# Kernel tuning notes

Hardware: AMD Instinct MI355X
Metric: run time of the kernel (lower is better)

The kernel has to match this reference:

```python
import jax, jax.numpy as jnp
import numpy as np

B, N, L = 2, 2048, 2048
DQ, DKV, H, WF = 1024, 1024, 16, 4
HD = DQ // H
EPS = 1e-5


def _ln(x, g, b):
    m = jnp.mean(x, axis=-1, keepdims=True)
    v = jnp.mean(jnp.square(x - m), axis=-1, keepdims=True)
    return (x - m) * jax.lax.rsqrt(v + EPS) * g + b


def setup_inputs() -> dict:
    key = jax.random.key(0)
    ks = jax.random.split(key, 12)
    s = 0.02
    return {
        "x_q": jax.random.normal(ks[0], (B, N, DQ), jnp.float32),
        "x_kv": jax.random.normal(ks[1], (B, L, DKV), jnp.float32),
        "qn_g": jnp.ones((DQ,), jnp.float32),
        "qn_b": jnp.zeros((DQ,), jnp.float32),
        "kvn_g": jnp.ones((DKV,), jnp.float32),
        "kvn_b": jnp.zeros((DKV,), jnp.float32),
        "Wq": jax.random.normal(ks[2], (DQ, DQ), jnp.float32) * s,
        "bq": jnp.zeros((DQ,), jnp.float32),
        "Wk": jax.random.normal(ks[3], (DQ, DKV), jnp.float32) * s,
        "bk": jnp.zeros((DQ,), jnp.float32),
        "Wv": jax.random.normal(ks[4], (DQ, DKV), jnp.float32) * s,
        "bv": jnp.zeros((DQ,), jnp.float32),
        "Wo": jax.random.normal(ks[5], (DQ, DQ), jnp.float32) * s,
        "bo": jnp.zeros((DQ,), jnp.float32),
        "n2_g": jnp.ones((DQ,), jnp.float32),
        "n2_b": jnp.zeros((DQ,), jnp.float32),
        "W1": jax.random.normal(ks[6], (WF * DQ, DQ), jnp.float32) * s,
        "b1": jnp.zeros((WF * DQ,), jnp.float32),
        "W2": jax.random.normal(ks[7], (DQ, WF * DQ), jnp.float32) * s,
        "b2": jnp.zeros((DQ,), jnp.float32),
    }


def reference(x_q, x_kv, qn_g, qn_b, kvn_g, kvn_b, Wq, bq, Wk, bk, Wv, bv,
              Wo, bo, n2_g, n2_b, W1, b1, W2, b2):
    # projections (torch Linear: x @ W.T + b)
    q = (_ln(x_q, qn_g, qn_b) @ Wq.T + bq).reshape(B, N, H, HD)
    kvn = _ln(x_kv, kvn_g, kvn_b)
    k = (kvn @ Wk.T + bk).reshape(B, L, H, HD)
    v = (kvn @ Wv.T + bv).reshape(B, L, H, HD)

    # attention with softmax-1: exp(s)/(1 + sum exp(s)), numerically stable
    scale = 1.0 / jnp.sqrt(jnp.float32(HD))
    s = jnp.einsum("bnhd,blhd->bhnl", q, k) * scale  # [B,H,N,L]
    m = jnp.max(s, axis=-1, keepdims=True)
    m = jnp.maximum(m, 0.0)  # include the implicit zero logit of softmax-1
    p = jnp.exp(s - m)
    denom = jnp.sum(p, axis=-1, keepdims=True) + jnp.exp(-m)
    attn = p / denom
    attn_out = jnp.einsum("bhnl,blhd->bnhd", attn, v).reshape(B, N, DQ)

    # residual + out proj
    x = x_q + (attn_out @ Wo.T + bo)
    # residual MLP (GELU, exact/erf as torch nn.GELU default)
    h = jax.nn.gelu(_ln(x, n2_g, n2_b) @ W1.T + b1, approximate=False)
    x = x + (h @ W2.T + b2)
    return x
```

## Files before the change

kernel.cpp:

```cpp
#include <hip/hip_runtime.h>
#include <hip/hip_bf16.h>
#include <stdint.h>

#define DEV __device__ __forceinline__

typedef unsigned short ushort_t;
typedef __attribute__((ext_vector_type(8))) short bf16x8;
typedef __attribute__((ext_vector_type(4))) float f32x4;

DEV ushort_t f2bf(float f) {
  union { float f; uint32_t u; } v; v.f = f;
  uint32_t r = v.u + 0x7FFFu + ((v.u >> 16) & 1u);
  return (ushort_t)(r >> 16);
}

DEV void gload_lds16(const void* gp, void* lp) {
  __builtin_amdgcn_global_load_lds(
      (__attribute__((address_space(1))) void*)(void*)(uintptr_t)gp,
      (__attribute__((address_space(3))) void*)lp, 16, 0, 0);
}

__global__ __launch_bounds__(256) void cvt_all(
    const float* __restrict__ Wq, const float* __restrict__ Wk,
    const float* __restrict__ Wv, const float* __restrict__ Wo,
    const float* __restrict__ W1, const float* __restrict__ W2,
    ushort_t* __restrict__ WqB, ushort_t* __restrict__ WKVB,
    ushort_t* __restrict__ WoB, ushort_t* __restrict__ W1B,
    ushort_t* __restrict__ W2B) {
  int i = blockIdx.x * 256 + threadIdx.x;
  const float* src; ushort_t* dst; int j;
  if (i < 262144)            { src = Wq; dst = WqB;           j = i; }
  else if (i < 524288)       { src = Wk; dst = WKVB;          j = i - 262144; }
  else if (i < 786432)       { src = Wv; dst = WKVB + 1048576; j = i - 524288; }
  else if (i < 1048576)      { src = Wo; dst = WoB;           j = i - 786432; }
  else if (i < 2097152)      { src = W1; dst = W1B;           j = i - 1048576; }
  else                       { src = W2; dst = W2B;           j = i - 2097152; }
  float4 v = ((const float4*)src)[j];
  ushort4 o;
  o.x = f2bf(v.x); o.y = f2bf(v.y); o.z = f2bf(v.z); o.w = f2bf(v.w);
  ((ushort4*)dst)[j] = o;
}

DEV void ln_row(const float* __restrict__ x, const float* __restrict__ g,
                const float* __restrict__ be, ushort_t* __restrict__ out, int row) {
  const int t = threadIdx.x;
  const float4 v = ((const float4*)(x + (size_t)row * 1024))[t];
  float s = v.x + v.y + v.z + v.w;
  float sq = v.x * v.x + v.y * v.y + v.z * v.z + v.w * v.w;
#pragma unroll
  for (int d = 1; d < 64; d <<= 1) { s += __shfl_xor(s, d); sq += __shfl_xor(sq, d); }
  __shared__ float sm[8];
  const int w = t >> 6, lane = t & 63;
  if (lane == 0) { sm[w * 2] = s; sm[w * 2 + 1] = sq; }
  __syncthreads();
  s = sm[0] + sm[2] + sm[4] + sm[6];
  sq = sm[1] + sm[3] + sm[5] + sm[7];
  const float mean = s * (1.f / 1024.f);
  const float var = sq * (1.f / 1024.f) - mean * mean;
  const float rstd = rsqrtf(var + 1e-5f);
  const float4 gv = ((const float4*)g)[t];
  const float4 bv = ((const float4*)be)[t];
  ushort4 o;
  o.x = f2bf((v.x - mean) * rstd * gv.x + bv.x);
  o.y = f2bf((v.y - mean) * rstd * gv.y + bv.y);
  o.z = f2bf((v.z - mean) * rstd * gv.z + bv.z);
  o.w = f2bf((v.w - mean) * rstd * gv.w + bv.w);
  ((ushort4*)(out + (size_t)row * 1024))[t] = o;
}

__global__ __launch_bounds__(256) void ln_bf16(const float* __restrict__ x,
                                               const float* __restrict__ g,
                                               const float* __restrict__ be,
                                               ushort_t* __restrict__ out) {
  ln_row(x, g, be, out, blockIdx.x);
}

__global__ __launch_bounds__(256) void ln_fused(
    const float* __restrict__ x_q, const float* __restrict__ x_kv,
    const float* __restrict__ qg, const float* __restrict__ qb,
    const float* __restrict__ kg, const float* __restrict__ kb,
    ushort_t* __restrict__ oq, ushort_t* __restrict__ okv) {
  const int r = blockIdx.x;
  if (r < 4096) ln_row(x_q, qg, qb, oq, r);
  else ln_row(x_kv, kg, kb, okv, r - 4096);
}

enum { EPI_BF16 = 0, EPI_KV = 1, EPI_RESID = 2, EPI_GELU = 3 };

template <int TN, int EPI>
__global__ __launch_bounds__(256, 2) void gemm_bt(
    const ushort_t* __restrict__ A,
    const ushort_t* __restrict__ Wb,
    const float* __restrict__ bias,
    const float* __restrict__ bias2,
    const float* __restrict__ resid,
    void* __restrict__ outp, void* __restrict__ outp2,
    int M, int N, int K) {
  constexpr int NI = (TN == 128) ? 4 : 2;
  __shared__ ushort_t As[128 * 64];
  __shared__ ushort_t Bs[TN * 64];
  const int t = threadIdx.x;
  const int w = t >> 6, lane = t & 63;
  const int qd = lane >> 4, ql = lane & 15;
  const int m0 = blockIdx.y * 128, n0 = blockIdx.x * TN;
  const int wm = (TN == 128) ? (w >> 1) * 64 : w * 32;
  const int wn = (TN == 128) ? (w & 1) * 64 : 0;
  const int sw = ql & 7;

  f32x4 acc[NI][4] = {};

  for (int k0 = 0; k0 < K; k0 += 64) {
#pragma unroll
    for (int p = 0; p < 4; p++) {
      int n = p * 256 + t, row = n >> 3, c = (n & 7) ^ (row & 7);
      gload_lds16(A + (size_t)(m0 + row) * K + k0 + c * 8, &As[n * 8]);
    }
#pragma unroll
    for (int p = 0; p < TN / 32; p++) {
      int n = p * 256 + t, row = n >> 3, c = (n & 7) ^ (row & 7);
      gload_lds16(Wb + (size_t)(n0 + row) * K + k0 + c * 8, &Bs[n * 8]);
    }
    __syncthreads();
#pragma unroll
    for (int ks = 0; ks < 2; ks++) {
      bf16x8 af[NI], bf[4];
#pragma unroll
      for (int i = 0; i < NI; i++)
        af[i] = *(const bf16x8*)&As[(wm + i * 16 + ql) * 64 + ((ks * 4 + qd) ^ sw) * 8];
#pragma unroll
      for (int j = 0; j < 4; j++)
        bf[j] = *(const bf16x8*)&Bs[(wn + j * 16 + ql) * 64 + ((ks * 4 + qd) ^ sw) * 8];
#pragma unroll
      for (int i = 0; i < NI; i++)
#pragma unroll
        for (int j = 0; j < 4; j++)
          acc[i][j] = __builtin_amdgcn_mfma_f32_16x16x32_bf16(af[i], bf[j], acc[i][j], 0, 0, 0);
    }
    __syncthreads();
  }

#pragma unroll
  for (int i = 0; i < NI; i++) {
    const int mr = m0 + wm + i * 16 + qd * 4;
#pragma unroll
    for (int j = 0; j < 4; j++) {
      const int col = n0 + wn + j * 16 + ql;
      f32x4 v = acc[i][j];
      if constexpr (EPI == EPI_BF16) {
        const float bb = bias[col];
        ushort_t* o = (ushort_t*)outp;
#pragma unroll
        for (int r = 0; r < 4; r++) o[(size_t)(mr + r) * N + col] = f2bf(v[r] + bb);
      } else if constexpr (EPI == EPI_KV) {
        if (col < 1024) {
          const float bb = bias[col];
          ushort_t* o = (ushort_t*)outp;
#pragma unroll
          for (int r = 0; r < 4; r++) o[(size_t)(mr + r) * 1024 + col] = f2bf(v[r] + bb);
        } else {
          const int vc = col - 1024;
          const float bb = bias2[vc];
          const int h = vc >> 6, d = vc & 63;
          const int b = mr >> 11, l0 = mr & 2047;
          ushort4 pk;
          pk.x = f2bf(v[0] + bb); pk.y = f2bf(v[1] + bb);
          pk.z = f2bf(v[2] + bb); pk.w = f2bf(v[3] + bb);
          *(ushort4*)((ushort_t*)outp2 + ((((size_t)b * 16 + h) * 64 + d) * 2048 + l0)) = pk;
        }
      } else if constexpr (EPI == EPI_RESID) {
        const float bb = bias[col];
        float* o = (float*)outp;
#pragma unroll
        for (int r = 0; r < 4; r++) {
          size_t idx = (size_t)(mr + r) * N + col;
          o[idx] = resid[idx] + v[r] + bb;
        }
      } else {
        const float bb = bias[col];
        ushort_t* o = (ushort_t*)outp;
#pragma unroll
        for (int r = 0; r < 4; r++) {
          float x = v[r] + bb;
          float gx = 0.5f * x * (1.0f + erff(x * 0.70710678118654752f));
          o[(size_t)(mr + r) * N + col] = f2bf(gx);
        }
      }
    }
  }
}

__global__ __launch_bounds__(256, 2) void flash_attn(const ushort_t* __restrict__ Qg,
                                                     const ushort_t* __restrict__ Kg,
                                                     const ushort_t* __restrict__ VTg,
                                                     ushort_t* __restrict__ Og) {
  __shared__ ushort_t Qs[128 * 64];
  __shared__ ushort_t Ks[2][64 * 64];
  __shared__ ushort_t Vs[2][64 * 64];
  __shared__ ushort_t Ps[128 * 64];
  const int t = threadIdx.x, w = t >> 6, lane = t & 63;
  const int qd = lane >> 4, ql = lane & 15;
  const int bh = blockIdx.y, b = bh >> 4, h = bh & 15;
  const int n0 = blockIdx.x * 128;
  const ushort_t* Qp = Qg + ((size_t)b * 2048 + n0) * 1024 + h * 64;
  const ushort_t* Kp = Kg + (size_t)b * 2048 * 1024 + h * 64;
  const ushort_t* Vp = VTg + (size_t)bh * 64 * 2048;
  const int sw = ql & 7;

#pragma unroll
  for (int p = 0; p < 4; p++) {
    int n = p * 256 + t, row = n >> 3, c = (n & 7) ^ (row & 7);
    gload_lds16(Qp + (size_t)row * 1024 + c * 8, &Qs[n * 8]);
  }
#pragma unroll
  for (int p = 0; p < 2; p++) {
    int n = p * 256 + t, row = n >> 3, c = (n & 7) ^ (row & 7);
    gload_lds16(Kp + (size_t)row * 1024 + c * 8, &Ks[0][n * 8]);
    gload_lds16(Vp + (size_t)row * 2048 + c * 8, &Vs[0][n * 8]);
  }
  __syncthreads();

  bf16x8 aq[2][2];
#pragma unroll
  for (int i = 0; i < 2; i++)
#pragma unroll
    for (int ks = 0; ks < 2; ks++)
      aq[i][ks] = *(const bf16x8*)&Qs[(w * 32 + i * 16 + ql) * 64 + ((ks * 4 + qd) ^ sw) * 8];

  f32x4 accO[2][4] = {};
  float lro[2][4] = {};

  int cur = 0;
  for (int lt = 0; lt < 32; ++lt) {
    if (lt + 1 < 32) {
      const int l0n = (lt + 1) * 64;
#pragma unroll
      for (int p = 0; p < 2; p++) {
        int n = p * 256 + t, row = n >> 3, c = (n & 7) ^ (row & 7);
        gload_lds16(Kp + (size_t)(l0n + row) * 1024 + c * 8, &Ks[1 ^ cur][n * 8]);
        gload_lds16(Vp + (size_t)row * 2048 + l0n + c * 8, &Vs[1 ^ cur][n * 8]);
      }
    }
    const ushort_t* Kc = Ks[cur];
    const ushort_t* Vc = Vs[cur];

    f32x4 accS[2][4] = {};
#pragma unroll
    for (int ks = 0; ks < 2; ks++) {
      bf16x8 bk[4];
#pragma unroll
      for (int j = 0; j < 4; j++)
        bk[j] = *(const bf16x8*)&Kc[(j * 16 + ql) * 64 + ((ks * 4 + qd) ^ sw) * 8];
#pragma unroll
      for (int i = 0; i < 2; i++)
#pragma unroll
        for (int j = 0; j < 4; j++)
          accS[i][j] = __builtin_amdgcn_mfma_f32_16x16x32_bf16(aq[i][ks], bk[j], accS[i][j], 0, 0, 0);
    }

#pragma unroll
    for (int i = 0; i < 2; i++)
#pragma unroll
      for (int j = 0; j < 4; j++)
#pragma unroll
        for (int r = 0; r < 4; r++) {
          float p_ = __expf(accS[i][j][r] * 0.125f);
          accS[i][j][r] = p_;
          lro[i][r] += p_;
        }

#pragma unroll
    for (int i = 0; i < 2; i++)
#pragma unroll
      for (int j = 0; j < 4; j++) {
        const int col = j * 16 + ql;
#pragma unroll
        for (int r = 0; r < 4; r++) {
          const int row = w * 32 + i * 16 + qd * 4 + r;
          Ps[row * 64 + (((col >> 3) ^ (row & 7)) * 8) + (col & 7)] = f2bf(accS[i][j][r]);
        }
      }

#pragma unroll
    for (int ks = 0; ks < 2; ks++) {
      bf16x8 ap[2], bv[4];
#pragma unroll
      for (int i = 0; i < 2; i++)
        ap[i] = *(const bf16x8*)&Ps[(w * 32 + i * 16 + ql) * 64 + ((ks * 4 + qd) ^ sw) * 8];
#pragma unroll
      for (int jo = 0; jo < 4; jo++)
        bv[jo] = *(const bf16x8*)&Vc[(jo * 16 + ql) * 64 + ((ks * 4 + qd) ^ sw) * 8];
#pragma unroll
      for (int i = 0; i < 2; i++)
#pragma unroll
        for (int jo = 0; jo < 4; jo++)
          accO[i][jo] = __builtin_amdgcn_mfma_f32_16x16x32_bf16(ap[i], bv[jo], accO[i][jo], 0, 0, 0);
    }

    __syncthreads();
    cur ^= 1;
  }

#pragma unroll
  for (int i = 0; i < 2; i++)
#pragma unroll
    for (int r = 0; r < 4; r++) {
      float l = lro[i][r];
#pragma unroll
      for (int d = 1; d < 16; d <<= 1) l += __shfl_xor(l, d);
      const float inv = 1.0f / (l + 1.0f);
      const int row = n0 + w * 32 + i * 16 + qd * 4 + r;
#pragma unroll
      for (int jo = 0; jo < 4; jo++)
        Og[((size_t)b * 2048 + row) * 1024 + h * 64 + jo * 16 + ql] =
            f2bf(accO[i][jo][r] * inv);
    }
}

extern "C" void kernel_launch(void* const* d_in, const int* in_sizes, int n_in,
                              void* d_out, int out_size, void* d_ws, size_t ws_size,
                              hipStream_t stream) {
  const float* x_q = (const float*)d_in[0];
  const float* x_kv = (const float*)d_in[1];
  const float* qn_g = (const float*)d_in[2];
  const float* qn_b = (const float*)d_in[3];
  const float* kvn_g = (const float*)d_in[4];
  const float* kvn_b = (const float*)d_in[5];
  const float* Wq = (const float*)d_in[6];
  const float* bq = (const float*)d_in[7];
  const float* Wk = (const float*)d_in[8];
  const float* bk = (const float*)d_in[9];
  const float* Wv = (const float*)d_in[10];
  const float* bv = (const float*)d_in[11];
  const float* Wo = (const float*)d_in[12];
  const float* bo = (const float*)d_in[13];
  const float* n2_g = (const float*)d_in[14];
  const float* n2_b = (const float*)d_in[15];
  const float* W1 = (const float*)d_in[16];
  const float* b1 = (const float*)d_in[17];
  const float* W2 = (const float*)d_in[18];
  const float* b2 = (const float*)d_in[19];

  char* ws = (char*)d_ws;
  const size_t MB = 1ull << 20;
  ushort_t* WqB = (ushort_t*)(ws + 0 * MB);
  ushort_t* WKVB = (ushort_t*)(ws + 2 * MB);
  ushort_t* WoB = (ushort_t*)(ws + 6 * MB);
  ushort_t* W1B = (ushort_t*)(ws + 8 * MB);
  ushort_t* W2B = (ushort_t*)(ws + 16 * MB);
  ushort_t* LNQ = (ushort_t*)(ws + 24 * MB);
  ushort_t* LNKV = (ushort_t*)(ws + 32 * MB);
  ushort_t* Qb = (ushort_t*)(ws + 40 * MB);
  ushort_t* Kb = (ushort_t*)(ws + 48 * MB);
  ushort_t* VTb = (ushort_t*)(ws + 56 * MB);
  ushort_t* AOb = (ushort_t*)(ws + 64 * MB);
  float* Xf = (float*)(ws + 72 * MB);
  ushort_t* LN2 = (ushort_t*)(ws + 88 * MB);
  ushort_t* Hb = (ushort_t*)(ws + 24 * MB);

  cvt_all<<<12288, 256, 0, stream>>>(Wq, Wk, Wv, Wo, W1, W2, WqB, WKVB, WoB, W1B, W2B);
  ln_fused<<<8192, 256, 0, stream>>>(x_q, x_kv, qn_g, qn_b, kvn_g, kvn_b, LNQ, LNKV);

  gemm_bt<64, EPI_BF16><<<dim3(16, 32), 256, 0, stream>>>(
      LNQ, WqB, bq, nullptr, nullptr, Qb, nullptr, 4096, 1024, 1024);
  gemm_bt<128, EPI_KV><<<dim3(16, 32), 256, 0, stream>>>(
      LNKV, WKVB, bk, bv, nullptr, Kb, VTb, 4096, 2048, 1024);

  flash_attn<<<dim3(16, 32), 256, 0, stream>>>(Qb, Kb, VTb, AOb);

  gemm_bt<64, EPI_RESID><<<dim3(16, 32), 256, 0, stream>>>(
      AOb, WoB, bo, nullptr, x_q, Xf, nullptr, 4096, 1024, 1024);
  ln_bf16<<<4096, 256, 0, stream>>>(Xf, n2_g, n2_b, LN2);
  gemm_bt<128, EPI_GELU><<<dim3(32, 32), 256, 0, stream>>>(
      LN2, W1B, b1, nullptr, nullptr, Hb, nullptr, 4096, 4096, 1024);
  gemm_bt<64, EPI_RESID><<<dim3(16, 32), 256, 0, stream>>>(
      Hb, W2B, b2, nullptr, Xf, (float*)d_out, nullptr, 4096, 1024, 4096);
}
```

Baseline: 401.8 us.

## Use hardware bf16 pack, fold softmax scale into Q, share LDS, raise occupancy

Replaces the software bf16 rounding with the v_cvt_pk_bf16_f32 instruction and packs pairs of results into 32-bit stores. The softmax scale times log2(e) is folded into the Q projection epilogue, so attention can use a raw exp2. Attention reuses the Q staging buffer for P to cut LDS use, and launch bounds rise from 2 to 3 blocks per CU. Global load pointers are precomputed and advanced each iteration instead of recomputing addresses. The occupancy target may force register spills, and rounding Q to bf16 after scaling slightly changes numerics.

```diff
diff --git a/kernel.cpp b/kernel.cpp
--- a/kernel.cpp
+++ b/kernel.cpp
@@ -8,11 +8,12 @@
 typedef __attribute__((ext_vector_type(8))) short bf16x8;
 typedef __attribute__((ext_vector_type(4))) float f32x4;
 
-DEV ushort_t f2bf(float f) {
-  union { float f; uint32_t u; } v; v.f = f;
-  uint32_t r = v.u + 0x7FFFu + ((v.u >> 16) & 1u);
-  return (ushort_t)(r >> 16);
-}
+DEV uint32_t f2bf2(float lo, float hi) {
+  uint32_t d;
+  asm("v_cvt_pk_bf16_f32 %0, %1, %2" : "=v"(d) : "v"(lo), "v"(hi));
+  return d;
+}
+DEV ushort_t f2bf(float f) { return (ushort_t)f2bf2(f, f); }
 
 DEV void gload_lds16(const void* gp, void* lp) {
   __builtin_amdgcn_global_load_lds(
@@ -36,9 +37,8 @@
   else if (i < 2097152)      { src = W1; dst = W1B;           j = i - 1048576; }
   else                       { src = W2; dst = W2B;           j = i - 2097152; }
   float4 v = ((const float4*)src)[j];
-  ushort4 o;
-  o.x = f2bf(v.x); o.y = f2bf(v.y); o.z = f2bf(v.z); o.w = f2bf(v.w);
-  ((ushort4*)dst)[j] = o;
+  uint2 o; o.x = f2bf2(v.x, v.y); o.y = f2bf2(v.z, v.w);
+  ((uint2*)dst)[j] = o;
 }
 
 DEV void ln_row(const float* __restrict__ x, const float* __restrict__ g,
@@ -60,12 +60,10 @@
   const float rstd = rsqrtf(var + 1e-5f);
   const float4 gv = ((const float4*)g)[t];
   const float4 bv = ((const float4*)be)[t];
-  ushort4 o;
-  o.x = f2bf((v.x - mean) * rstd * gv.x + bv.x);
-  o.y = f2bf((v.y - mean) * rstd * gv.y + bv.y);
-  o.z = f2bf((v.z - mean) * rstd * gv.z + bv.z);
-  o.w = f2bf((v.w - mean) * rstd * gv.w + bv.w);
-  ((ushort4*)(out + (size_t)row * 1024))[t] = o;
+  uint2 o;
+  o.x = f2bf2((v.x - mean) * rstd * gv.x + bv.x, (v.y - mean) * rstd * gv.y + bv.y);
+  o.y = f2bf2((v.z - mean) * rstd * gv.z + bv.z, (v.w - mean) * rstd * gv.w + bv.w);
+  ((uint2*)(out + (size_t)row * 1024))[t] = o;
 }
 
 __global__ __launch_bounds__(256) void ln_bf16(const float* __restrict__ x,
@@ -88,15 +86,16 @@
 enum { EPI_BF16 = 0, EPI_KV = 1, EPI_RESID = 2, EPI_GELU = 3 };
 
 template <int TN, int EPI>
-__global__ __launch_bounds__(256, 2) void gemm_bt(
+__global__ __launch_bounds__(256, 3) void gemm_bt(
     const ushort_t* __restrict__ A,
     const ushort_t* __restrict__ Wb,
     const float* __restrict__ bias,
     const float* __restrict__ bias2,
     const float* __restrict__ resid,
     void* __restrict__ outp, void* __restrict__ outp2,
-    int M, int N, int K) {
+    int M, int N, int K, float oscale) {
   constexpr int NI = (TN == 128) ? 4 : 2;
+  constexpr int NB = TN / 32;
   __shared__ ushort_t As[128 * 64];
   __shared__ ushort_t Bs[TN * 64];
   const int t = threadIdx.x;
@@ -107,18 +106,31 @@
   const int wn = (TN == 128) ? (w & 1) * 64 : 0;
   const int sw = ql & 7;
 
+  const ushort_t* pa[4];
+#pragma unroll
+  for (int p = 0; p < 4; p++) {
+    int n = p * 256 + t, row = n >> 3, c = (n & 7) ^ (row & 7);
+    pa[p] = A + (size_t)(m0 + row) * K + c * 8;
+  }
+  const ushort_t* pb[NB];
+#pragma unroll
+  for (int p = 0; p < NB; p++) {
+    int n = p * 256 + t, row = n >> 3, c = (n & 7) ^ (row & 7);
+    pb[p] = Wb + (size_t)(n0 + row) * K + c * 8;
+  }
+
   f32x4 acc[NI][4] = {};
 
   for (int k0 = 0; k0 < K; k0 += 64) {
 #pragma unroll
     for (int p = 0; p < 4; p++) {
-      int n = p * 256 + t, row = n >> 3, c = (n & 7) ^ (row & 7);
-      gload_lds16(A + (size_t)(m0 + row) * K + k0 + c * 8, &As[n * 8]);
-    }
-#pragma unroll
-    for (int p = 0; p < TN / 32; p++) {
-      int n = p * 256 + t, row = n >> 3, c = (n & 7) ^ (row & 7);
-      gload_lds16(Wb + (size_t)(n0 + row) * K + k0 + c * 8, &Bs[n * 8]);
+      gload_lds16(pa[p], &As[(p * 256 + t) * 8]);
+      pa[p] += 64;
+    }
+#pragma unroll
+    for (int p = 0; p < NB; p++) {
+      gload_lds16(pb[p], &Bs[(p * 256 + t) * 8]);
+      pb[p] += 64;
     }
     __syncthreads();
 #pragma unroll
@@ -150,7 +162,7 @@
         const float bb = bias[col];
         ushort_t* o = (ushort_t*)outp;
 #pragma unroll
-        for (int r = 0; r < 4; r++) o[(size_t)(mr + r) * N + col] = f2bf(v[r] + bb);
+        for (int r = 0; r < 4; r++) o[(size_t)(mr + r) * N + col] = f2bf((v[r] + bb) * oscale);
       } else if constexpr (EPI == EPI_KV) {
         if (col < 1024) {
           const float bb = bias[col];
@@ -162,10 +174,10 @@
           const float bb = bias2[vc];
           const int h = vc >> 6, d = vc & 63;
           const int b = mr >> 11, l0 = mr & 2047;
-          ushort4 pk;
-          pk.x = f2bf(v[0] + bb); pk.y = f2bf(v[1] + bb);
-          pk.z = f2bf(v[2] + bb); pk.w = f2bf(v[3] + bb);
-          *(ushort4*)((ushort_t*)outp2 + ((((size_t)b * 16 + h) * 64 + d) * 2048 + l0)) = pk;
+          uint2 pk;
+          pk.x = f2bf2(v[0] + bb, v[1] + bb);
+          pk.y = f2bf2(v[2] + bb, v[3] + bb);
+          *(uint2*)((ushort_t*)outp2 + ((((size_t)b * 16 + h) * 64 + d) * 2048 + l0)) = pk;
         }
       } else if constexpr (EPI == EPI_RESID) {
         const float bb = bias[col];
@@ -189,14 +201,13 @@
   }
 }
 
-__global__ __launch_bounds__(256, 2) void flash_attn(const ushort_t* __restrict__ Qg,
+__global__ __launch_bounds__(256, 3) void flash_attn(const ushort_t* __restrict__ Qg,
                                                      const ushort_t* __restrict__ Kg,
                                                      const ushort_t* __restrict__ VTg,
                                                      ushort_t* __restrict__ Og) {
-  __shared__ ushort_t Qs[128 * 64];
+  __shared__ ushort_t QPs[128 * 64];
   __shared__ ushort_t Ks[2][64 * 64];
   __shared__ ushort_t Vs[2][64 * 64];
-  __shared__ ushort_t Ps[128 * 64];
   const int t = threadIdx.x, w = t >> 6, lane = t & 63;
   const int qd = lane >> 4, ql = lane & 15;
   const int bh = blockIdx.y, b = bh >> 4, h = bh & 15;
@@ -206,16 +217,27 @@
   const ushort_t* Vp = VTg + (size_t)bh * 64 * 2048;
   const int sw = ql & 7;
 
+  const ushort_t* kp2[2];
+  const ushort_t* vp2[2];
+#pragma unroll
+  for (int p = 0; p < 2; p++) {
+    int n = p * 256 + t, row = n >> 3, c = (n & 7) ^ (row & 7);
+    kp2[p] = Kp + (size_t)row * 1024 + c * 8;
+    vp2[p] = Vp + (size_t)row * 2048 + c * 8;
+  }
+
 #pragma unroll
   for (int p = 0; p < 4; p++) {
     int n = p * 256 + t, row = n >> 3, c = (n & 7) ^ (row & 7);
-    gload_lds16(Qp + (size_t)row * 1024 + c * 8, &Qs[n * 8]);
+    gload_lds16(Qp + (size_t)row * 1024 + c * 8, &QPs[n * 8]);
   }
 #pragma unroll
   for (int p = 0; p < 2; p++) {
-    int n = p * 256 + t, row = n >> 3, c = (n & 7) ^ (row & 7);
-    gload_lds16(Kp + (size_t)row * 1024 + c * 8, &Ks[0][n * 8]);
-    gload_lds16(Vp + (size_t)row * 2048 + c * 8, &Vs[0][n * 8]);
+    int n = p * 256 + t;
+    gload_lds16(kp2[p], &Ks[0][n * 8]);
+    gload_lds16(vp2[p], &Vs[0][n * 8]);
+    kp2[p] += 64 * 1024;
+    vp2[p] += 64;
   }
   __syncthreads();
 
@@ -224,7 +246,8 @@
   for (int i = 0; i < 2; i++)
 #pragma unroll
     for (int ks = 0; ks < 2; ks++)
-      aq[i][ks] = *(const bf16x8*)&Qs[(w * 32 + i * 16 + ql) * 64 + ((ks * 4 + qd) ^ sw) * 8];
+      aq[i][ks] = *(const bf16x8*)&QPs[(w * 32 + i * 16 + ql) * 64 + ((ks * 4 + qd) ^ sw) * 8];
+  __syncthreads();
 
   f32x4 accO[2][4] = {};
   float lro[2][4] = {};
@@ -232,12 +255,13 @@
   int cur = 0;
   for (int lt = 0; lt < 32; ++lt) {
     if (lt + 1 < 32) {
-      const int l0n = (lt + 1) * 64;
 #pragma unroll
       for (int p = 0; p < 2; p++) {
-        int n = p * 256 + t, row = n >> 3, c = (n & 7) ^ (row & 7);
-        gload_lds16(Kp + (size_t)(l0n + row) * 1024 + c * 8, &Ks[1 ^ cur][n * 8]);
-        gload_lds16(Vp + (size_t)row * 2048 + l0n + c * 8, &Vs[1 ^ cur][n * 8]);
+        int n = p * 256 + t;
+        gload_lds16(kp2[p], &Ks[1 ^ cur][n * 8]);
+        gload_lds16(vp2[p], &Vs[1 ^ cur][n * 8]);
+        kp2[p] += 64 * 1024;
+        vp2[p] += 64;
       }
     }
     const ushort_t* Kc = Ks[cur];
@@ -263,7 +287,7 @@
       for (int j = 0; j < 4; j++)
 #pragma unroll
         for (int r = 0; r < 4; r++) {
-          float p_ = __expf(accS[i][j][r] * 0.125f);
+          float p_ = __builtin_amdgcn_exp2f(accS[i][j][r]);
           accS[i][j][r] = p_;
           lro[i][r] += p_;
         }
@@ -276,7 +300,7 @@
 #pragma unroll
         for (int r = 0; r < 4; r++) {
           const int row = w * 32 + i * 16 + qd * 4 + r;
-          Ps[row * 64 + (((col >> 3) ^ (row & 7)) * 8) + (col & 7)] = f2bf(accS[i][j][r]);
+          QPs[row * 64 + (((col >> 3) ^ (row & 7)) * 8) + (col & 7)] = f2bf(accS[i][j][r]);
         }
       }
 
@@ -285,7 +309,7 @@
       bf16x8 ap[2], bv[4];
 #pragma unroll
       for (int i = 0; i < 2; i++)
-        ap[i] = *(const bf16x8*)&Ps[(w * 32 + i * 16 + ql) * 64 + ((ks * 4 + qd) ^ sw) * 8];
+        ap[i] = *(const bf16x8*)&QPs[(w * 32 + i * 16 + ql) * 64 + ((ks * 4 + qd) ^ sw) * 8];
 #pragma unroll
       for (int jo = 0; jo < 4; jo++)
         bv[jo] = *(const bf16x8*)&Vc[(jo * 16 + ql) * 64 + ((ks * 4 + qd) ^ sw) * 8];
@@ -357,21 +381,23 @@
   ushort_t* LN2 = (ushort_t*)(ws + 88 * MB);
   ushort_t* Hb = (ushort_t*)(ws + 24 * MB);
 
+  const float QSCALE = 0.18033688011112042f;
+
   cvt_all<<<12288, 256, 0, stream>>>(Wq, Wk, Wv, Wo, W1, W2, WqB, WKVB, WoB, W1B, W2B);
   ln_fused<<<8192, 256, 0, stream>>>(x_q, x_kv, qn_g, qn_b, kvn_g, kvn_b, LNQ, LNKV);
 
   gemm_bt<64, EPI_BF16><<<dim3(16, 32), 256, 0, stream>>>(
-      LNQ, WqB, bq, nullptr, nullptr, Qb, nullptr, 4096, 1024, 1024);
+      LNQ, WqB, bq, nullptr, nullptr, Qb, nullptr, 4096, 1024, 1024, QSCALE);
   gemm_bt<128, EPI_KV><<<dim3(16, 32), 256, 0, stream>>>(
-      LNKV, WKVB, bk, bv, nullptr, Kb, VTb, 4096, 2048, 1024);
+      LNKV, WKVB, bk, bv, nullptr, Kb, VTb, 4096, 2048, 1024, 1.0f);
 
   flash_attn<<<dim3(16, 32), 256, 0, stream>>>(Qb, Kb, VTb, AOb);
 
   gemm_bt<64, EPI_RESID><<<dim3(16, 32), 256, 0, stream>>>(
-      AOb, WoB, bo, nullptr, x_q, Xf, nullptr, 4096, 1024, 1024);
+      AOb, WoB, bo, nullptr, x_q, Xf, nullptr, 4096, 1024, 1024, 1.0f);
   ln_bf16<<<4096, 256, 0, stream>>>(Xf, n2_g, n2_b, LN2);
   gemm_bt<128, EPI_GELU><<<dim3(32, 32), 256, 0, stream>>>(
-      LN2, W1B, b1, nullptr, nullptr, Hb, nullptr, 4096, 4096, 1024);
+      LN2, W1B, b1, nullptr, nullptr, Hb, nullptr, 4096, 4096, 1024, 1.0f);
   gemm_bt<64, EPI_RESID><<<dim3(16, 32), 256, 0, stream>>>(
-      Hb, W2B, b2, nullptr, Xf, (float*)d_out, nullptr, 4096, 1024, 4096);
-}
+      Hb, W2B, b2, nullptr, Xf, (float*)d_out, nullptr, 4096, 1024, 4096, 1.0f);
+}
```

After: 381.7 us. -5.0%, faster.
